# Kernel tuning notes

Hardware: AMD Instinct MI355X
Metric: run time of the kernel (lower is better)

The kernel has to match this reference:

```python
import jax, jax.numpy as jnp
import numpy as np

E = 96   # embed dim (MultiheadAttention(96, 6))
H = 6    # heads
DH = E // H  # head dim = 16


def setup_inputs() -> dict:
    key = jax.random.key(0)
    ks = jax.random.split(key, 6)
    N, G = 4096, 64
    feats = jax.random.normal(ks[0], (N, E), jnp.float32)
    group = jax.random.randint(ks[1], (N,), 0, G)
    s = 1.0 / np.sqrt(E)
    # nn.MultiheadAttention packed in_proj [3E, E] and out_proj [E, E]
    w_in = jax.random.uniform(ks[2], (3 * E, E), jnp.float32, -s, s)
    b_in = jnp.zeros((3 * E,), jnp.float32)
    w_out = jax.random.uniform(ks[3], (E, E), jnp.float32, -s, s)
    b_out = jnp.zeros((E,), jnp.float32)
    # classifier Linear(96, 1)
    w_cls = jax.random.uniform(ks[4], (1, E), jnp.float32, -s, s)
    b_cls = jnp.zeros((1,), jnp.float32)
    return {"feats": feats, "group": group, "w_in": w_in, "b_in": b_in,
            "w_out": w_out, "b_out": b_out, "w_cls": w_cls, "b_cls": b_cls}


def reference(feats, group, w_in, b_in, w_out, b_out, w_cls, b_cls):
    # Per-group self-attention: softmax restricted to rows of the same group
    # is mathematically identical to running MHA on each group separately.
    N = feats.shape[0]
    qkv = feats @ w_in.T + b_in                     # [N, 3E]
    q, k, v = jnp.split(qkv, 3, axis=-1)            # each [N, E]
    to_heads = lambda t: t.reshape(N, H, DH).transpose(1, 0, 2)  # [H, N, DH]
    q = to_heads(q) * (1.0 / np.sqrt(DH))
    k = to_heads(k)
    v = to_heads(v)
    scores = jnp.einsum('hnd,hmd->hnm', q, k)       # [H, N, N]
    same_group = group[:, None] == group[None, :]   # [N, N] (diag always True)
    scores = jnp.where(same_group[None], scores, jnp.float32(-1e9))
    attn = jax.nn.softmax(scores, axis=-1)
    out = jnp.einsum('hnm,hmd->hnd', attn, v)       # [H, N, DH]
    out = out.transpose(1, 0, 2).reshape(N, E)
    out = out @ w_out.T + b_out                     # out_proj
    logits = out @ w_cls.T + b_cls                  # [N, 1]
    return jax.nn.sigmoid(logits)[:, 0]             # cluster_scores [N]
```

## Files before the change

kernel.cpp:

```cpp
#include <hip/hip_runtime.h>
#include <math.h>

#define N 4096
#define E 96
#define H 6
#define DH 16
#define G 64
#define CMAX 128
#define KSTR 19
#define NW 8
#define NT 512

__global__ __launch_bounds__(NT, 6) void fused_kernel(const float* __restrict__ feats,
                                                      const int* __restrict__ grp,
                                                      const float* __restrict__ w_in,
                                                      const float* __restrict__ b_in,
                                                      const float* __restrict__ w_out,
                                                      const float* __restrict__ w_cls,
                                                      float* __restrict__ part) {
    __shared__ float wl[48 * 100];
    __shared__ float kh[CMAX * KSTR];
    __shared__ float vh[CMAX * KSTR];
    __shared__ float qh[64 * KSTR];
    __shared__ float ps[NW * CMAX];
    __shared__ int   bucket[CMAX];
    __shared__ unsigned long long smask[64];
    __shared__ int   scount[64];
    __shared__ int   soffs[64];
    __shared__ float wfh[DH];
    __shared__ int   scnt;

    int g  = blockIdx.x & 63;
    int hh = blockIdx.x >> 6;
    int h  = hh >> 1;
    int hb = hh & 1;
    int tid = threadIdx.x, lane = tid & 63, wv = tid >> 6;

    #pragma unroll
    for (int c8 = 0; c8 < 8; ++c8) {
        int cc = wv * 8 + c8;
        bool mt = (grp[(cc << 6) + lane] == g);
        unsigned long long mask = __ballot(mt);
        if (lane == 0) { smask[cc] = mask; scount[cc] = __popcll(mask); }
    }

    for (int idx = tid; idx < 48 * 24; idx += NT) {
        int ci = idx / 24, j = idx % 24;
        int pp = ci >> 4, dd = ci & 15;
        int gcol = pp * E + h * DH + dd;
        *(float4*)(wl + ci * 100 + j * 4) = *(const float4*)(w_in + gcol * E + j * 4);
    }

    if (wv == 7) {
        int dd = lane & 15, u4 = lane >> 4;
        float s = 0.f;
        for (int u = u4 * 24; u < u4 * 24 + 24; ++u)
            s += w_cls[u] * w_out[u * E + h * DH + dd];
        s += __shfl_xor(s, 16, 64);
        s += __shfl_xor(s, 32, 64);
        if (lane < DH) wfh[lane] = s;
    }
    __syncthreads();

    if (wv == 0) {
        int v = scount[lane];
        int x = v;
        #pragma unroll
        for (int o = 1; o < 64; o <<= 1) {
            int y = __shfl_up(x, o, 64);
            if (lane >= o) x += y;
        }
        soffs[lane] = x - v;
        if (lane == 63) scnt = x;
    } else {
        for (int idx = tid - 64; idx < CMAX * KSTR; idx += NT - 64) vh[idx] = 0.f;
    }
    __syncthreads();

    int cnt = scnt; if (cnt > CMAX) cnt = CMAX;

    #pragma unroll
    for (int c8 = 0; c8 < 8; ++c8) {
        int cc = wv * 8 + c8;
        unsigned long long mask = smask[cc];
        if ((mask >> lane) & 1ULL) {
            int pos = soffs[cc] + __popcll(mask & ((1ULL << lane) - 1ULL));
            if (pos < CMAX) bucket[pos] = (cc << 6) + lane;
        }
    }
    __syncthreads();

    int d = tid & 15, rr = tid >> 4;
    float bk = b_in[E + h * DH + d];
    float bv = b_in[2 * E + h * DH + d];
    const float4* wk  = (const float4*)(wl + (16 + d) * 100);
    const float4* wvp = (const float4*)(wl + (32 + d) * 100);
    #pragma unroll
    for (int p = 0; p < 4; ++p) {
        int s = rr + 32 * p;
        if (s < cnt) {
            const float4* fp = (const float4*)(feats + bucket[s] * E);
            float sk = 0.f, sv = 0.f;
            #pragma unroll
            for (int e4 = 0; e4 < 24; ++e4) {
                float4 f = fp[e4];
                float4 b = wk[e4], c = wvp[e4];
                sk += f.x*b.x + f.y*b.y + f.z*b.z + f.w*b.w;
                sv += f.x*c.x + f.y*c.y + f.z*c.z + f.w*c.w;
            }
            kh[s * KSTR + d] = sk + bk;
            vh[s * KSTR + d] = sv + bv;
        }
    }

    float bq = b_in[h * DH + d];
    const float4* wq = (const float4*)(wl + d * 100);
    #pragma unroll
    for (int p = 0; p < 2; ++p) {
        int j = rr + 32 * p;
        int r = 2 * j + hb;
        if (r < cnt) {
            const float4* fp = (const float4*)(feats + bucket[r] * E);
            float sq = 0.f;
            #pragma unroll
            for (int e4 = 0; e4 < 24; ++e4) {
                float4 f = fp[e4];
                float4 a = wq[e4];
                sq += f.x*a.x + f.y*a.y + f.z*a.z + f.w*a.w;
            }
            qh[j * KSTR + d] = (sq + bq) * 0.25f;
        }
    }
    __syncthreads();

    for (int j = wv; 2 * j + hb < cnt; j += NW) {
        int r = 2 * j + hb;
        float qv[16];
        #pragma unroll
        for (int e = 0; e < 16; ++e) qv[e] = qh[j * KSTR + e];

        float a0 = 0.f;
        #pragma unroll
        for (int e = 0; e < 16; ++e) a0 += qv[e] * kh[lane * KSTR + e];
        float s0 = (lane < cnt) ? a0 : -INFINITY;
        float s1 = -INFINITY;
        if (cnt > 64) {
            float a1 = 0.f;
            #pragma unroll
            for (int e = 0; e < 16; ++e) a1 += qv[e] * kh[(64 + lane) * KSTR + e];
            s1 = (64 + lane < cnt) ? a1 : -INFINITY;
        }

        float m = fmaxf(s0, s1);
        #pragma unroll
        for (int o = 32; o >= 1; o >>= 1) m = fmaxf(m, __shfl_xor(m, o, 64));
        float p0 = __expf(s0 - m);
        float p1 = (cnt > 64) ? __expf(s1 - m) : 0.f;
        float l = p0 + p1;
        #pragma unroll
        for (int o = 32; o >= 1; o >>= 1) l += __shfl_xor(l, o, 64);
        ps[wv * CMAX + lane] = p0;
        ps[wv * CMAX + 64 + lane] = p1;

        int mm4 = lane >> 4, dd = lane & 15;
        float acc = 0.f;
        #pragma unroll
        for (int k = 0; k < 16; ++k) {
            int m2 = mm4 + 4 * k;
            acc += ps[wv * CMAX + m2] * vh[m2 * KSTR + dd];
        }
        if (cnt > 64) {
            #pragma unroll
            for (int k = 16; k < 32; ++k) {
                int m2 = mm4 + 4 * k;
                acc += ps[wv * CMAX + m2] * vh[m2 * KSTR + dd];
            }
        }
        acc += __shfl_xor(acc, 16, 64);
        acc += __shfl_xor(acc, 32, 64);

        float pt = (acc / l) * wfh[dd];
        pt += __shfl_xor(pt, 1, 64);
        pt += __shfl_xor(pt, 2, 64);
        pt += __shfl_xor(pt, 4, 64);
        pt += __shfl_xor(pt, 8, 64);
        if (lane == 0) part[bucket[r] * 8 + h] = pt;
    }
}

__global__ __launch_bounds__(512) void sigmoid_kernel(const float* __restrict__ part,
                                                      const float* __restrict__ w_cls,
                                                      const float* __restrict__ b_out,
                                                      const float* __restrict__ b_cls,
                                                      float* __restrict__ out) {
    __shared__ float sbias;
    int tid = threadIdx.x;
    if (tid < 64) {
        float s = w_cls[tid] * b_out[tid];
        if (tid < 32) s += w_cls[tid + 64] * b_out[tid + 64];
        #pragma unroll
        for (int o = 32; o >= 1; o >>= 1) s += __shfl_xor(s, o, 64);
        if (tid == 0) sbias = s + b_cls[0];
    }
    __syncthreads();
    int i = blockIdx.x * 512 + tid;
    const float4* p = (const float4*)(part + i * 8);
    float4 u = p[0], v = p[1];
    float s = u.x + u.y + u.z + u.w + v.x + v.y + sbias;
    out[i] = 1.f / (1.f + __expf(-s));
}

extern "C" void kernel_launch(void* const* d_in, const int* in_sizes, int n_in,
                              void* d_out, int out_size, void* d_ws, size_t ws_size,
                              hipStream_t stream) {
    const float* feats = (const float*)d_in[0];
    const int*   grp   = (const int*)  d_in[1];
    const float* w_in  = (const float*)d_in[2];
    const float* b_in  = (const float*)d_in[3];
    const float* w_out = (const float*)d_in[4];
    const float* b_out = (const float*)d_in[5];
    const float* w_cls = (const float*)d_in[6];
    const float* b_cls = (const float*)d_in[7];
    float* out = (float*)d_out;

    float* part = (float*)d_ws;

    fused_kernel<<<G * H * 2, NT, 0, stream>>>(feats, grp, w_in, b_in, w_out, w_cls, part);
    sigmoid_kernel<<<N / 512, 512, 0, stream>>>(part, w_cls, b_out, b_cls, out);
}
```

Measured before the change: 110.4 us.

## Compute per-group QKV projection with bf16 MFMA from LDS-staged features

Result: faster. 100.6 us (-8.9%).

```diff
diff --git a/kernel.cpp b/kernel.cpp
--- a/kernel.cpp
+++ b/kernel.cpp
@@ -8,17 +8,31 @@
 #define G 64
 #define CMAX 128
 #define KSTR 19
+#define FSTR 104
 #define NW 8
 #define NT 512
 
-__global__ __launch_bounds__(NT, 6) void fused_kernel(const float* __restrict__ feats,
+typedef __attribute__((ext_vector_type(8))) short short8;
+typedef __attribute__((ext_vector_type(4))) float f32x4;
+
+static __device__ __forceinline__ unsigned short f2bf(float f) {
+    unsigned u = __builtin_bit_cast(unsigned, f);
+    return (unsigned short)((u + 0x7fffu + ((u >> 16) & 1u)) >> 16);
+}
+static __device__ __forceinline__ unsigned pack2(float lo, float hi) {
+    return (unsigned)f2bf(lo) | ((unsigned)f2bf(hi) << 16);
+}
+
+__global__ __launch_bounds__(NT, 4) void fused_kernel(const float* __restrict__ feats,
                                                       const int* __restrict__ grp,
                                                       const float* __restrict__ w_in,
                                                       const float* __restrict__ b_in,
                                                       const float* __restrict__ w_out,
                                                       const float* __restrict__ w_cls,
                                                       float* __restrict__ part) {
-    __shared__ float wl[48 * 100];
+    __shared__ short fA[CMAX * FSTR];
+    __shared__ short wB[48 * FSTR];
+    __shared__ float bia[48];
     __shared__ float kh[CMAX * KSTR];
     __shared__ float vh[CMAX * KSTR];
     __shared__ float qh[64 * KSTR];
@@ -44,14 +58,21 @@
         if (lane == 0) { smask[cc] = mask; scount[cc] = __popcll(mask); }
     }
 
-    for (int idx = tid; idx < 48 * 24; idx += NT) {
-        int ci = idx / 24, j = idx % 24;
-        int pp = ci >> 4, dd = ci & 15;
-        int gcol = pp * E + h * DH + dd;
-        *(float4*)(wl + ci * 100 + j * 4) = *(const float4*)(w_in + gcol * E + j * 4);
-    }
-
-    if (wv == 7) {
+    if (tid < 384) {
+        int row = tid >> 3, seg = tid & 7;
+        int gcol = (row >> 4) * E + h * DH + (row & 15);
+        const float4* src = (const float4*)(w_in + gcol * E + seg * 12);
+        unsigned* dst = (unsigned*)(wB + row * FSTR + seg * 12);
+        #pragma unroll
+        for (int t = 0; t < 3; ++t) {
+            float4 v = src[t];
+            dst[2 * t]     = pack2(v.x, v.y);
+            dst[2 * t + 1] = pack2(v.z, v.w);
+        }
+    } else if (tid < 432) {
+        int c = tid - 384;
+        bia[c] = b_in[(c >> 4) * E + h * DH + (c & 15)];
+    } else if (wv == 7) {
         int dd = lane & 15, u4 = lane >> 4;
         float s = 0.f;
         for (int u = u4 * 24; u < u4 * 24 + 24; ++u)
@@ -90,45 +111,47 @@
     }
     __syncthreads();
 
-    int d = tid & 15, rr = tid >> 4;
-    float bk = b_in[E + h * DH + d];
-    float bv = b_in[2 * E + h * DH + d];
-    const float4* wk  = (const float4*)(wl + (16 + d) * 100);
-    const float4* wvp = (const float4*)(wl + (32 + d) * 100);
-    #pragma unroll
-    for (int p = 0; p < 4; ++p) {
-        int s = rr + 32 * p;
-        if (s < cnt) {
-            const float4* fp = (const float4*)(feats + bucket[s] * E);
-            float sk = 0.f, sv = 0.f;
-            #pragma unroll
-            for (int e4 = 0; e4 < 24; ++e4) {
-                float4 f = fp[e4];
-                float4 b = wk[e4], c = wvp[e4];
-                sk += f.x*b.x + f.y*b.y + f.z*b.z + f.w*b.w;
-                sv += f.x*c.x + f.y*c.y + f.z*c.z + f.w*c.w;
+    {
+        int srow = tid >> 2, sq = tid & 3;
+        if (srow < cnt) {
+            const float4* src = (const float4*)(feats + bucket[srow] * E + sq * 24);
+            unsigned* dst = (unsigned*)(fA + srow * FSTR + sq * 24);
+            #pragma unroll
+            for (int t = 0; t < 6; ++t) {
+                float4 v = src[t];
+                dst[2 * t]     = pack2(v.x, v.y);
+                dst[2 * t + 1] = pack2(v.z, v.w);
             }
-            kh[s * KSTR + d] = sk + bk;
-            vh[s * KSTR + d] = sv + bv;
-        }
-    }
-
-    float bq = b_in[h * DH + d];
-    const float4* wq = (const float4*)(wl + d * 100);
-    #pragma unroll
-    for (int p = 0; p < 2; ++p) {
-        int j = rr + 32 * p;
-        int r = 2 * j + hb;
-        if (r < cnt) {
-            const float4* fp = (const float4*)(feats + bucket[r] * E);
-            float sq = 0.f;
-            #pragma unroll
-            for (int e4 = 0; e4 < 24; ++e4) {
-                float4 f = fp[e4];
-                float4 a = wq[e4];
-                sq += f.x*a.x + f.y*a.y + f.z*a.z + f.w*a.w;
+        }
+    }
+    __syncthreads();
+
+    {
+        int lr = lane & 15, kg = lane >> 4;
+        int njobs = ((cnt + 15) >> 4) * 3;
+        for (int jj = wv; jj < njobs; jj += NW) {
+            int rt = jj / 3;
+            int ct = jj - rt * 3;
+            const short* ab = fA + (rt * 16 + lr) * FSTR + kg * 8;
+            const short* bb = wB + (ct * 16 + lr) * FSTR + kg * 8;
+            f32x4 acc = {0.f, 0.f, 0.f, 0.f};
+            acc = __builtin_amdgcn_mfma_f32_16x16x32_bf16(*(const short8*)(ab),
+                                                          *(const short8*)(bb), acc, 0, 0, 0);
+            acc = __builtin_amdgcn_mfma_f32_16x16x32_bf16(*(const short8*)(ab + 32),
+                                                          *(const short8*)(bb + 32), acc, 0, 0, 0);
+            acc = __builtin_amdgcn_mfma_f32_16x16x32_bf16(*(const short8*)(ab + 64),
+                                                          *(const short8*)(bb + 64), acc, 0, 0, 0);
+            float bias = bia[ct * 16 + lr];
+            #pragma unroll
+            for (int r = 0; r < 4; ++r) {
+                int row = rt * 16 + kg * 4 + r;
+                if (row < cnt) {
+                    float v = acc[r] + bias;
+                    if (ct == 1)      kh[row * KSTR + lr] = v;
+                    else if (ct == 2) vh[row * KSTR + lr] = v;
+                    else if ((row & 1) == hb) qh[(row >> 1) * KSTR + lr] = v * 0.25f;
+                }
             }
-            qh[j * KSTR + d] = (sq + bq) * 0.25f;
         }
     }
     __syncthreads();
```
